# Optimization experiments

Hardware: AMD Instinct MI355X
Metric: run time of the kernel (lower is better)

Reference implementation:

```python
import jax, jax.numpy as jnp
import numpy as np

N, C, H, W = 16, 512, 64, 64
C_BAR, C_HAT = 64, 256


def max_pool2(t):
    # t: [n, c, h, w] -> [n, c, h//2, w//2] via 2x2 max pool
    n, c, h, w = t.shape
    return t.reshape(n, c, h // 2, 2, w // 2, 2).max(axis=(3, 5))


def setup_inputs() -> dict:
    key = jax.random.key(0)
    ks = jax.random.split(key, 6)
    x = jax.random.normal(ks[0], (N, C, H, W), dtype=jnp.float32)
    # 1x1 conv weights stored as [out_channels, in_channels]
    w_theta = jax.random.normal(ks[1], (C_BAR, C), dtype=jnp.float32) * 0.02
    w_phi = jax.random.normal(ks[2], (C_BAR, C), dtype=jnp.float32) * 0.02
    w_g = jax.random.normal(ks[3], (C_HAT, C), dtype=jnp.float32) * 0.02
    w_o = jax.random.normal(ks[4], (C, C_HAT), dtype=jnp.float32) * 0.02
    # gamma initialized to zero in the module; use a small nonzero value so the
    # attention path contributes to the output (and to gradients).
    gamma = jnp.full((1,), 0.1, dtype=jnp.float32)
    return {"x": x, "w_theta": w_theta, "w_phi": w_phi, "w_g": w_g,
            "w_o": w_o, "gamma": gamma}


def reference(x, w_theta, w_phi, w_g, w_o, gamma):
    n, c, h, w = x.shape
    hw, hw4 = h * w, (h * w) // 4
    # 1x1 conv projections (pure channel GEMMs)
    g_x = jnp.einsum('nchw,oc->nohw', x, w_g)          # [n, c_hat, h, w]
    g_x = max_pool2(g_x).reshape(n, -1, hw4)            # [n, c_hat, hw/4]
    phi_x = jnp.einsum('nchw,oc->nohw', x, w_phi)       # [n, c_bar, h, w]
    phi_x = max_pool2(phi_x).reshape(n, -1, hw4)        # [n, c_bar, hw/4]
    theta_x = jnp.einsum('nchw,oc->nohw', x, w_theta).reshape(n, -1, hw)  # [n, c_bar, hw]
    # bmm -> softmax -> bmm
    scores = jnp.einsum('nds,ndt->nst', theta_x, phi_x)  # [n, hw, hw/4]
    attn = jax.nn.softmax(scores, axis=-1)
    y = jnp.einsum('ndt,nst->nds', g_x, attn)            # [n, c_hat, hw]
    y = y.reshape(n, -1, h, w)
    o = jnp.einsum('nchw,oc->nohw', y, w_o)              # [n, c, h, w]
    return gamma[0] * o + x
```

## Files before the change

kernel.cpp:

```cpp
#include <hip/hip_runtime.h>
#include <stdint.h>

typedef unsigned short u16;
typedef u16   us4 __attribute__((ext_vector_type(4)));
typedef u16   us8 __attribute__((ext_vector_type(8)));
typedef __bf16 bf8 __attribute__((ext_vector_type(8)));
typedef float f4  __attribute__((ext_vector_type(4)));

__device__ __forceinline__ u16 f2bf(float f) {
    uint32_t u = __builtin_bit_cast(uint32_t, f);
    uint32_t r = (u + 0x7fffu + ((u >> 16) & 1u)) >> 16;
    return (u16)r;
}
__device__ __forceinline__ float bf2f(u16 s) {
    uint32_t u = ((uint32_t)s) << 16;
    return __builtin_bit_cast(float, u);
}
__device__ __forceinline__ f4 mfma16(bf8 a, bf8 b, f4 c) {
    return __builtin_amdgcn_mfma_f32_16x16x32_bf16(a, b, c, 0, 0, 0);
}
__device__ __forceinline__ u16 max4bf(u16 a, u16 b, u16 c, u16 d) {
    float m = fmaxf(fmaxf(bf2f(a), bf2f(b)), fmaxf(bf2f(c), bf2f(d)));
    return f2bf(m);
}

__global__ __launch_bounds__(256) void xt_kernel(
    const float* __restrict__ x, u16* __restrict__ Xt)
{
    const int s0 = blockIdx.x * 64, c0 = blockIdx.y * 64, n = blockIdx.z;
    const int tid = threadIdx.x;
    __shared__ u16 lds[64 * 72];

    {
        int c_loc = tid & 63, s_seg = (tid >> 6) * 16;
        const float* src = x + ((size_t)n * 512 + c0 + c_loc) * 4096 + s0 + s_seg;
        for (int i4 = 0; i4 < 4; i4++) {
            float4 f = *(const float4*)(src + i4 * 4);
            int s = s_seg + i4 * 4;
            lds[(s + 0) * 72 + c_loc] = f2bf(f.x);
            lds[(s + 1) * 72 + c_loc] = f2bf(f.y);
            lds[(s + 2) * 72 + c_loc] = f2bf(f.z);
            lds[(s + 3) * 72 + c_loc] = f2bf(f.w);
        }
    }
    __syncthreads();
    {
        int s_loc = tid >> 2, c_seg = (tid & 3) * 16;
        u16* dst = Xt + ((size_t)n * 4096 + s0 + s_loc) * 512 + c0 + c_seg;
        *(us8*)(dst)     = *(const us8*)&lds[s_loc * 72 + c_seg];
        *(us8*)(dst + 8) = *(const us8*)&lds[s_loc * 72 + c_seg + 8];
    }
}

__global__ __launch_bounds__(256) void wconv_kernel(
    const float* __restrict__ w_theta, const float* __restrict__ w_phi,
    const float* __restrict__ w_g, const float* __restrict__ w_o,
    u16* __restrict__ Wall_bf, u16* __restrict__ Wo_bf)
{
    int base = (blockIdx.x * 256 + threadIdx.x) * 4;
    const float* src; u16* dst;
    if (base < 32768)       { src = w_theta + base;          dst = Wall_bf + base; }
    else if (base < 65536)  { src = w_phi + (base - 32768);  dst = Wall_bf + base; }
    else if (base < 196608) { src = w_g + (base - 65536);    dst = Wall_bf + base; }
    else                    { src = w_o + (base - 196608);   dst = Wo_bf + (base - 196608); }
    float4 f = *(const float4*)src;
    us4 v; v[0] = f2bf(f.x); v[1] = f2bf(f.y); v[2] = f2bf(f.z); v[3] = f2bf(f.w);
    *(us4*)dst = v;
}

__global__ __launch_bounds__(256) void projT_gemm(
    const u16* __restrict__ Xt, const u16* __restrict__ Wall_bf,
    u16* __restrict__ PT)
{
    const int s0 = blockIdx.x * 128;
    const int r0 = blockIdx.y * 128;
    const int nb = blockIdx.z;
    const int tid = threadIdx.x;
    const int wave = tid >> 6, lane = tid & 63;
    const int quad = lane >> 4, l15 = lane & 15;
    const int wm = (wave >> 1) * 64, wn = (wave & 1) * 64;

    __shared__ u16 a_lds[128 * 40];
    __shared__ u16 b_lds[128 * 40];

    f4 acc[4][4];
    f4 z = {0.f, 0.f, 0.f, 0.f};
    for (int i = 0; i < 4; i++) for (int j = 0; j < 4; j++) acc[i][j] = z;

    const u16* Abase = Xt + ((size_t)nb * 4096 + s0) * 512;
    const int m = tid >> 1, kseg = (tid & 1) * 16;

    for (int k0 = 0; k0 < 512; k0 += 32) {
        *(us8*)&a_lds[m * 40 + kseg]     = *(const us8*)(Abase + (size_t)m * 512 + k0 + kseg);
        *(us8*)&a_lds[m * 40 + kseg + 8] = *(const us8*)(Abase + (size_t)m * 512 + k0 + kseg + 8);
        *(us8*)&b_lds[m * 40 + kseg]     = *(const us8*)(Wall_bf + (size_t)(r0 + m) * 512 + k0 + kseg);
        *(us8*)&b_lds[m * 40 + kseg + 8] = *(const us8*)(Wall_bf + (size_t)(r0 + m) * 512 + k0 + kseg + 8);
        __syncthreads();
        bf8 af[4], bfr[4];
        for (int i = 0; i < 4; i++)
            af[i]  = __builtin_bit_cast(bf8, *(const us8*)&a_lds[(wm + i*16 + l15)*40 + quad*8]);
        for (int j = 0; j < 4; j++)
            bfr[j] = __builtin_bit_cast(bf8, *(const us8*)&b_lds[(wn + j*16 + l15)*40 + quad*8]);
        for (int i = 0; i < 4; i++)
            for (int j = 0; j < 4; j++)
                acc[i][j] = mfma16(af[i], bfr[j], acc[i][j]);
        __syncthreads();
    }
    for (int i = 0; i < 4; i++) {
        int s_idx = s0 + wm + i * 16 + quad * 4;
        for (int rr = 0; rr < 4; rr++) {
            u16* dst = PT + ((size_t)nb * 4096 + s_idx + rr) * 384 + r0 + wn + l15;
            for (int j = 0; j < 4; j++)
                dst[j * 16] = f2bf(acc[i][j][rr]);
        }
    }
}

__global__ __launch_bounds__(256) void phi_pool2(
    const u16* __restrict__ PT, u16* __restrict__ phiT)
{
    int n = blockIdx.y, t0 = blockIdx.x * 64;
    int tid = threadIdx.x;
    int t_loc = tid >> 2, d0 = (tid & 3) * 16;
    int t = t0 + t_loc;
    int h2 = t >> 5, w2 = t & 31;
    int s00 = h2 * 128 + w2 * 2;
    const u16* base = PT + ((size_t)n * 4096) * 384 + 64 + d0;
    us8 r[4][2];
    int soff[4] = {s00, s00 + 1, s00 + 64, s00 + 65};
    for (int p = 0; p < 4; p++) {
        r[p][0] = *(const us8*)(base + (size_t)soff[p] * 384);
        r[p][1] = *(const us8*)(base + (size_t)soff[p] * 384 + 8);
    }
    us8 o0, o1;
    for (int i = 0; i < 8; i++) {
        o0[i] = max4bf(r[0][0][i], r[1][0][i], r[2][0][i], r[3][0][i]);
        o1[i] = max4bf(r[0][1][i], r[1][1][i], r[2][1][i], r[3][1][i]);
    }
    u16* dst = phiT + ((size_t)n * 1024 + t) * 64 + d0;
    *(us8*)dst = o0;
    *(us8*)(dst + 8) = o1;
}

__global__ __launch_bounds__(256) void g_poolT(
    const u16* __restrict__ PT, u16* __restrict__ gP)
{
    int t0 = blockIdx.x * 64, d0 = blockIdx.y * 64, n = blockIdx.z;
    int tid = threadIdx.x;
    __shared__ u16 lds[64 * 72];

    {
        int t_loc = tid & 63, dseg = (tid >> 6) * 16;
        int t = t0 + t_loc;
        int h2 = t >> 5, w2 = t & 31;
        int s00 = h2 * 128 + w2 * 2;
        const u16* base = PT + ((size_t)n * 4096) * 384 + 128 + d0 + dseg;
        us8 r[4][2];
        int soff[4] = {s00, s00 + 1, s00 + 64, s00 + 65};
        for (int p = 0; p < 4; p++) {
            r[p][0] = *(const us8*)(base + (size_t)soff[p] * 384);
            r[p][1] = *(const us8*)(base + (size_t)soff[p] * 384 + 8);
        }
        for (int i = 0; i < 8; i++) {
            lds[(dseg + i) * 72 + t_loc]     = max4bf(r[0][0][i], r[1][0][i], r[2][0][i], r[3][0][i]);
            lds[(dseg + 8 + i) * 72 + t_loc] = max4bf(r[0][1][i], r[1][1][i], r[2][1][i], r[3][1][i]);
        }
    }
    __syncthreads();
    {
        int d_loc = tid >> 2, t_seg = (tid & 3) * 16;
        u16* dst = gP + ((size_t)n * 256 + d0 + d_loc) * 1024 + t0 + t_seg;
        *(us8*)(dst)     = *(const us8*)&lds[d_loc * 72 + t_seg];
        *(us8*)(dst + 8) = *(const us8*)&lds[d_loc * 72 + t_seg + 8];
    }
}

__global__ __launch_bounds__(256) void attn_kernel(
    const u16* __restrict__ PT, const u16* __restrict__ phiT,
    const u16* __restrict__ gP, u16* __restrict__ yT)
{
    int n = blockIdx.y;
    int tid = threadIdx.x;
    int wave = tid >> 6, lane = tid & 63, quad = lane >> 4, l15 = lane & 15;
    int q0 = blockIdx.x * 64 + wave * 16;

    __shared__ u16 phi_lds[32 * 72];
    __shared__ u16 g_lds[256 * 40];
    __shared__ u16 p_lds[4][16 * 40];

    const u16* th = PT + ((size_t)n * 4096 + q0 + l15) * 384 + quad * 8;
    bf8 bth0 = __builtin_bit_cast(bf8, *(const us8*)(th));
    bf8 bth1 = __builtin_bit_cast(bf8, *(const us8*)(th + 32));

    const int t_loc = tid >> 3, d0 = (tid & 7) * 8;
    const u16* phi_src = phiT + ((size_t)n * 1024 + t_loc) * 64 + d0;
    const u16* g_src   = gP + ((size_t)n * 256 + tid) * 1024;

    f4 z = {0.f, 0.f, 0.f, 0.f};
    f4 acc[16];
    for (int b = 0; b < 16; b++) acc[b] = z;
    float lsum = 0.f;

    us8 pf_phi = *(const us8*)(phi_src);
    us8 pf_g0  = *(const us8*)(g_src + 0);
    us8 pf_g1  = *(const us8*)(g_src + 8);
    us8 pf_g2  = *(const us8*)(g_src + 16);
    us8 pf_g3  = *(const us8*)(g_src + 24);
    *(us8*)&phi_lds[t_loc * 72 + d0] = pf_phi;
    *(us8*)&g_lds[tid * 40 + 0]  = pf_g0;
    *(us8*)&g_lds[tid * 40 + 8]  = pf_g1;
    *(us8*)&g_lds[tid * 40 + 16] = pf_g2;
    *(us8*)&g_lds[tid * 40 + 24] = pf_g3;
    __syncthreads();

    for (int ci = 0; ci < 32; ci++) {
        int nc = (ci + 1 < 32) ? (ci + 1) : ci;
        pf_phi = *(const us8*)(phi_src + (size_t)nc * 2048);
        pf_g0  = *(const us8*)(g_src + nc * 32 + 0);
        pf_g1  = *(const us8*)(g_src + nc * 32 + 8);
        pf_g2  = *(const us8*)(g_src + nc * 32 + 16);
        pf_g3  = *(const us8*)(g_src + nc * 32 + 24);

        for (int tt = 0; tt < 32; tt += 16) {
            bf8 ap0 = __builtin_bit_cast(bf8, *(const us8*)&phi_lds[(tt + l15) * 72 + quad * 8]);
            bf8 ap1 = __builtin_bit_cast(bf8, *(const us8*)&phi_lds[(tt + l15) * 72 + 32 + quad * 8]);
            f4 s = mfma16(ap0, bth0, z);
            s = mfma16(ap1, bth1, s);
            us4 pk;
            float ps = 0.f;
            for (int rr = 0; rr < 4; rr++) {
                float p = __expf(s[rr]);
                ps += p;
                pk[rr] = f2bf(p);
            }
            lsum += ps;
            *(us4*)&p_lds[wave][l15 * 40 + tt + quad * 4] = pk;
        }
        bf8 bp = __builtin_bit_cast(bf8, *(const us8*)&p_lds[wave][l15 * 40 + quad * 8]);
        for (int b = 0; b < 16; b++) {
            bf8 ag = __builtin_bit_cast(bf8, *(const us8*)&g_lds[(b * 16 + l15) * 40 + quad * 8]);
            acc[b] = mfma16(ag, bp, acc[b]);
        }
        __syncthreads();
        *(us8*)&phi_lds[t_loc * 72 + d0] = pf_phi;
        *(us8*)&g_lds[tid * 40 + 0]  = pf_g0;
        *(us8*)&g_lds[tid * 40 + 8]  = pf_g1;
        *(us8*)&g_lds[tid * 40 + 16] = pf_g2;
        *(us8*)&g_lds[tid * 40 + 24] = pf_g3;
        __syncthreads();
    }

    float v = lsum;
    v += __shfl_xor(v, 16);
    v += __shfl_xor(v, 32);
    float inv = 1.0f / v;

    u16* dst = yT + ((size_t)n * 4096 + q0 + l15) * 256 + quad * 4;
    for (int b = 0; b < 16; b++) {
        us4 o;
        for (int rr = 0; rr < 4; rr++) o[rr] = f2bf(acc[b][rr] * inv);
        *(us4*)(dst + b * 16) = o;
    }
}

__global__ __launch_bounds__(256) void oproj_gemm(
    const u16* __restrict__ Wo_bf, const u16* __restrict__ yT,
    const float* __restrict__ x, const float* __restrict__ gamma,
    float* __restrict__ out)
{
    const int nt = blockIdx.x;
    const int mt = blockIdx.y;
    const int nb = blockIdx.z;
    const int tid = threadIdx.x;
    const int wave = tid >> 6, lane = tid & 63;
    const int quad = lane >> 4, l15 = lane & 15;
    const int wm = (wave >> 1) * 32, wn = (wave & 1) * 64;
    const int s0 = nt * 128;

    __shared__ u16 a_lds[64 * 40];
    __shared__ u16 b_lds[128 * 40];

    f4 acc[2][4];
    f4 z = {0.f, 0.f, 0.f, 0.f};
    for (int i = 0; i < 2; i++) for (int j = 0; j < 4; j++) acc[i][j] = z;

    for (int k0 = 0; k0 < 256; k0 += 32) {
        {
            int m = tid >> 2, kq = (tid & 3) * 8;
            *(us8*)&a_lds[m * 40 + kq] =
                *(const us8*)(Wo_bf + (size_t)(mt * 64 + m) * 256 + k0 + kq);
        }
        {
            int s_loc = tid >> 1, kq = (tid & 1) * 16;
            const u16* src = yT + ((size_t)nb * 4096 + s0 + s_loc) * 256 + k0 + kq;
            *(us8*)&b_lds[s_loc * 40 + kq]     = *(const us8*)(src);
            *(us8*)&b_lds[s_loc * 40 + kq + 8] = *(const us8*)(src + 8);
        }
        __syncthreads();
        bf8 af[2], bfr[4];
        for (int i = 0; i < 2; i++)
            af[i] = __builtin_bit_cast(bf8, *(const us8*)&a_lds[(wm + i*16 + l15)*40 + quad*8]);
        for (int j = 0; j < 4; j++)
            bfr[j] = __builtin_bit_cast(bf8, *(const us8*)&b_lds[(wn + j*16 + l15)*40 + quad*8]);
        for (int i = 0; i < 2; i++)
            for (int j = 0; j < 4; j++)
                acc[i][j] = mfma16(af[i], bfr[j], acc[i][j]);
        __syncthreads();
    }
    float g0 = gamma[0];
    for (int i = 0; i < 2; i++) {
        int c = mt * 64 + wm + i * 16 + quad * 4;
        for (int j = 0; j < 4; j++) {
            int s = s0 + wn + j * 16 + l15;
            for (int rr = 0; rr < 4; rr++) {
                size_t idx = ((size_t)nb * 512 + c + rr) * 4096 + s;
                out[idx] = g0 * acc[i][j][rr] + x[idx];
            }
        }
    }
}

extern "C" void kernel_launch(void* const* d_in, const int* in_sizes, int n_in,
                              void* d_out, int out_size, void* d_ws, size_t ws_size,
                              hipStream_t stream)
{
    (void)in_sizes; (void)n_in; (void)out_size; (void)ws_size;
    const float* x       = (const float*)d_in[0];
    const float* w_theta = (const float*)d_in[1];
    const float* w_phi   = (const float*)d_in[2];
    const float* w_g     = (const float*)d_in[3];
    const float* w_o     = (const float*)d_in[4];
    const float* gamma   = (const float*)d_in[5];
    float* out = (float*)d_out;

    char* ws = (char*)d_ws;
    u16* Xt      = (u16*)(ws);
    u16* yT      = (u16*)(ws);
    u16* phiT    = (u16*)(ws + 33554432);
    u16* gP      = (u16*)(ws + 35651584);
    u16* Wall_bf = (u16*)(ws + 67108864);
    u16* Wo_bf   = (u16*)(ws + 67502080);
    u16* PT      = (u16*)(ws + 67764224);

    xt_kernel  <<<dim3(64, 8, 16), 256, 0, stream>>>(x, Xt);
    wconv_kernel<<<320, 256, 0, stream>>>(w_theta, w_phi, w_g, w_o, Wall_bf, Wo_bf);
    projT_gemm <<<dim3(32, 3, 16), 256, 0, stream>>>(Xt, Wall_bf, PT);
    phi_pool2  <<<dim3(16, 16),    256, 0, stream>>>(PT, phiT);
    g_poolT    <<<dim3(16, 4, 16), 256, 0, stream>>>(PT, gP);
    attn_kernel<<<dim3(64, 16),    256, 0, stream>>>(PT, phiT, gP, yT);
    oproj_gemm <<<dim3(32, 8, 16), 256, 0, stream>>>(Wo_bf, yT, x, gamma, out);
}
```

Measured before the change: 435.4 us.

## Restructure attention kernel: register-direct phi/g loads, split C_hat across waves, XCD-aware tile remap

The attention kernel no longer stages phi and g tiles through LDS. Each lane loads its MFMA operands straight from global memory into registers, prefetched one chunk ahead. The output is now split so each wave owns 64 of the 256 g channels for all 64 queries, with P tiles shared across waves through a double-buffered LDS array. This needs one barrier per chunk instead of two, and row sums are exchanged through LDS at the end. Blocks are remapped from a 1D grid so consecutive tiles of the same batch land on the same XCD, meant to improve L2 reuse of phi and g. The risks are uncoalesced direct global loads with a 1024-element stride for g, and P exchange latency.

```diff
diff --git a/kernel.cpp b/kernel.cpp
--- a/kernel.cpp
+++ b/kernel.cpp
@@ -179,87 +179,100 @@
     const u16* __restrict__ PT, const u16* __restrict__ phiT,
     const u16* __restrict__ gP, u16* __restrict__ yT)
 {
-    int n = blockIdx.y;
-    int tid = threadIdx.x;
-    int wave = tid >> 6, lane = tid & 63, quad = lane >> 4, l15 = lane & 15;
-    int q0 = blockIdx.x * 64 + wave * 16;
-
-    __shared__ u16 phi_lds[32 * 72];
-    __shared__ u16 g_lds[256 * 40];
-    __shared__ u16 p_lds[4][16 * 40];
-
-    const u16* th = PT + ((size_t)n * 4096 + q0 + l15) * 384 + quad * 8;
+    const int orig = blockIdx.x;
+    const int tile = (orig & 7) * 128 + (orig >> 3);
+    const int n = tile >> 6;
+    const int q0b = (tile & 63) * 64;
+
+    const int tid = threadIdx.x;
+    const int wave = tid >> 6, lane = tid & 63, quad = lane >> 4, l15 = lane & 15;
+
+    __shared__ u16 p_lds[2][4][16 * 40];
+    __shared__ float qsum[64];
+
+    const u16* th = PT + ((size_t)n * 4096 + q0b + wave * 16 + l15) * 384 + quad * 8;
     bf8 bth0 = __builtin_bit_cast(bf8, *(const us8*)(th));
     bf8 bth1 = __builtin_bit_cast(bf8, *(const us8*)(th + 32));
 
-    const int t_loc = tid >> 3, d0 = (tid & 7) * 8;
-    const u16* phi_src = phiT + ((size_t)n * 1024 + t_loc) * 64 + d0;
-    const u16* g_src   = gP + ((size_t)n * 256 + tid) * 1024;
+    const u16* phi_base = phiT + ((size_t)n * 1024 + l15) * 64 + quad * 8;
+    const u16* g_base   = gP + ((size_t)n * 256 + wave * 64 + l15) * 1024 + quad * 8;
 
     f4 z = {0.f, 0.f, 0.f, 0.f};
-    f4 acc[16];
-    for (int b = 0; b < 16; b++) acc[b] = z;
+    f4 acc[4][4];
+    for (int i = 0; i < 4; i++) for (int j = 0; j < 4; j++) acc[i][j] = z;
     float lsum = 0.f;
 
-    us8 pf_phi = *(const us8*)(phi_src);
-    us8 pf_g0  = *(const us8*)(g_src + 0);
-    us8 pf_g1  = *(const us8*)(g_src + 8);
-    us8 pf_g2  = *(const us8*)(g_src + 16);
-    us8 pf_g3  = *(const us8*)(g_src + 24);
-    *(us8*)&phi_lds[t_loc * 72 + d0] = pf_phi;
-    *(us8*)&g_lds[tid * 40 + 0]  = pf_g0;
-    *(us8*)&g_lds[tid * 40 + 8]  = pf_g1;
-    *(us8*)&g_lds[tid * 40 + 16] = pf_g2;
-    *(us8*)&g_lds[tid * 40 + 24] = pf_g3;
-    __syncthreads();
+    us8 ph00 = *(const us8*)(phi_base);
+    us8 ph01 = *(const us8*)(phi_base + 32);
+    us8 ph10 = *(const us8*)(phi_base + 16 * 64);
+    us8 ph11 = *(const us8*)(phi_base + 16 * 64 + 32);
+    us8 gg0 = *(const us8*)(g_base);
+    us8 gg1 = *(const us8*)(g_base + 16 * 1024);
+    us8 gg2 = *(const us8*)(g_base + 32 * 1024);
+    us8 gg3 = *(const us8*)(g_base + 48 * 1024);
 
     for (int ci = 0; ci < 32; ci++) {
-        int nc = (ci + 1 < 32) ? (ci + 1) : ci;
-        pf_phi = *(const us8*)(phi_src + (size_t)nc * 2048);
-        pf_g0  = *(const us8*)(g_src + nc * 32 + 0);
-        pf_g1  = *(const us8*)(g_src + nc * 32 + 8);
-        pf_g2  = *(const us8*)(g_src + nc * 32 + 16);
-        pf_g3  = *(const us8*)(g_src + nc * 32 + 24);
-
-        for (int tt = 0; tt < 32; tt += 16) {
-            bf8 ap0 = __builtin_bit_cast(bf8, *(const us8*)&phi_lds[(tt + l15) * 72 + quad * 8]);
-            bf8 ap1 = __builtin_bit_cast(bf8, *(const us8*)&phi_lds[(tt + l15) * 72 + 32 + quad * 8]);
-            f4 s = mfma16(ap0, bth0, z);
-            s = mfma16(ap1, bth1, s);
-            us4 pk;
-            float ps = 0.f;
-            for (int rr = 0; rr < 4; rr++) {
-                float p = __expf(s[rr]);
-                ps += p;
-                pk[rr] = f2bf(p);
-            }
+        const int buf = ci & 1;
+        {
+            f4 s = mfma16(__builtin_bit_cast(bf8, ph00), bth0, z);
+            s = mfma16(__builtin_bit_cast(bf8, ph01), bth1, s);
+            us4 pk; float ps = 0.f;
+            for (int rr = 0; rr < 4; rr++) { float p = __expf(s[rr]); ps += p; pk[rr] = f2bf(p); }
             lsum += ps;
-            *(us4*)&p_lds[wave][l15 * 40 + tt + quad * 4] = pk;
-        }
-        bf8 bp = __builtin_bit_cast(bf8, *(const us8*)&p_lds[wave][l15 * 40 + quad * 8]);
-        for (int b = 0; b < 16; b++) {
-            bf8 ag = __builtin_bit_cast(bf8, *(const us8*)&g_lds[(b * 16 + l15) * 40 + quad * 8]);
-            acc[b] = mfma16(ag, bp, acc[b]);
-        }
-        __syncthreads();
-        *(us8*)&phi_lds[t_loc * 72 + d0] = pf_phi;
-        *(us8*)&g_lds[tid * 40 + 0]  = pf_g0;
-        *(us8*)&g_lds[tid * 40 + 8]  = pf_g1;
-        *(us8*)&g_lds[tid * 40 + 16] = pf_g2;
-        *(us8*)&g_lds[tid * 40 + 24] = pf_g3;
-        __syncthreads();
+            *(us4*)&p_lds[buf][wave][l15 * 40 + quad * 4] = pk;
+        }
+        {
+            f4 s = mfma16(__builtin_bit_cast(bf8, ph10), bth0, z);
+            s = mfma16(__builtin_bit_cast(bf8, ph11), bth1, s);
+            us4 pk; float ps = 0.f;
+            for (int rr = 0; rr < 4; rr++) { float p = __expf(s[rr]); ps += p; pk[rr] = f2bf(p); }
+            lsum += ps;
+            *(us4*)&p_lds[buf][wave][l15 * 40 + 16 + quad * 4] = pk;
+        }
+
+        __syncthreads();
+
+        bf8 ag0 = __builtin_bit_cast(bf8, gg0);
+        bf8 ag1 = __builtin_bit_cast(bf8, gg1);
+        bf8 ag2 = __builtin_bit_cast(bf8, gg2);
+        bf8 ag3 = __builtin_bit_cast(bf8, gg3);
+        {
+            const int nc = (ci + 1 < 32) ? ci + 1 : 31;
+            const u16* pb = phi_base + (size_t)nc * 2048;
+            ph00 = *(const us8*)(pb);
+            ph01 = *(const us8*)(pb + 32);
+            ph10 = *(const us8*)(pb + 16 * 64);
+            ph11 = *(const us8*)(pb + 16 * 64 + 32);
+            const u16* gb = g_base + nc * 32;
+            gg0 = *(const us8*)(gb);
+            gg1 = *(const us8*)(gb + 16 * 1024);
+            gg2 = *(const us8*)(gb + 32 * 1024);
+            gg3 = *(const us8*)(gb + 48 * 1024);
+        }
+
+        for (int j = 0; j < 4; j++) {
+            bf8 bp = __builtin_bit_cast(bf8, *(const us8*)&p_lds[buf][j][l15 * 40 + quad * 8]);
+            acc[0][j] = mfma16(ag0, bp, acc[0][j]);
+            acc[1][j] = mfma16(ag1, bp, acc[1][j]);
+            acc[2][j] = mfma16(ag2, bp, acc[2][j]);
+            acc[3][j] = mfma16(ag3, bp, acc[3][j]);
+        }
     }
 
     float v = lsum;
     v += __shfl_xor(v, 16);
     v += __shfl_xor(v, 32);
-    float inv = 1.0f / v;
-
-    u16* dst = yT + ((size_t)n * 4096 + q0 + l15) * 256 + quad * 4;
-    for (int b = 0; b < 16; b++) {
-        us4 o;
-        for (int rr = 0; rr < 4; rr++) o[rr] = f2bf(acc[b][rr] * inv);
-        *(us4*)(dst + b * 16) = o;
+    if (lane < 16) qsum[wave * 16 + lane] = v;
+    __syncthreads();
+
+    for (int j = 0; j < 4; j++) {
+        float invj = 1.0f / qsum[j * 16 + l15];
+        u16* dst = yT + ((size_t)n * 4096 + q0b + j * 16 + l15) * 256 + wave * 64 + quad * 4;
+        for (int i = 0; i < 4; i++) {
+            us4 o;
+            for (int rr = 0; rr < 4; rr++) o[rr] = f2bf(acc[i][j][rr] * invj);
+            *(us4*)(dst + i * 16) = o;
+        }
     }
 }
 
@@ -347,6 +360,6 @@
     projT_gemm <<<dim3(32, 3, 16), 256, 0, stream>>>(Xt, Wall_bf, PT);
     phi_pool2  <<<dim3(16, 16),    256, 0, stream>>>(PT, phiT);
     g_poolT    <<<dim3(16, 4, 16), 256, 0, stream>>>(PT, gP);
-    attn_kernel<<<dim3(64, 16),    256, 0, stream>>>(PT, phiT, gP, yT);
+    attn_kernel<<<dim3(1024),      256, 0, stream>>>(PT, phiT, gP, yT);
     oproj_gemm <<<dim3(32, 8, 16), 256, 0, stream>>>(Wo_bf, yT, x, gamma, out);
 }
```

After: 474.2 us. 8.9% more time.
